# Kernel tuning notes

Hardware: AMD Instinct MI355X
Metric: run time of the kernel (lower is better)

The kernel has to match this reference:

```python
import jax, jax.numpy as jnp
import numpy as np

RATIO = 2          # BigVGAN Activation1d up/down ratio
K_FILT = 12        # int(6 * ratio // 2) * 2
DILATIONS = (1, 3, 5)


def _kaiser_sinc_filter1d(cutoff, half_width, kernel_size):
    # Faithful port of BigVGAN's kaiser_sinc_filter1d (even kernel path).
    half_size = kernel_size // 2
    delta_f = 4.0 * half_width
    A = 2.285 * (half_size - 1) * np.pi * delta_f + 7.95
    if A > 50.0:
        beta = 0.1102 * (A - 8.7)
    elif A >= 21.0:
        beta = 0.5842 * (A - 21.0) ** 0.4 + 0.07886 * (A - 21.0)
    else:
        beta = 0.0
    window = np.kaiser(kernel_size, beta)              # periodic=False
    time = np.arange(-half_size, half_size) + 0.5       # even kernel size
    filt = 2.0 * cutoff * window * np.sinc(2.0 * cutoff * time)
    filt = filt / filt.sum()
    return jnp.asarray(filt, dtype=jnp.float32)

FILT = _kaiser_sinc_filter1d(0.5 / RATIO, 0.6 / RATIO, K_FILT)


def _depthwise1d(x, filt, stride, lhs_dilation, padding):
    # x: (B, T, C), filt: (k,) shared across channels (depthwise)
    C = x.shape[-1]
    kern = jnp.tile(filt[:, None, None], (1, 1, C))  # (k, 1, C)
    return jax.lax.conv_general_dilated(
        x, kern, window_strides=(stride,), padding=padding,
        lhs_dilation=(lhs_dilation,), feature_group_count=C,
        dimension_numbers=('NLC', 'LIO', 'NLC'))


def upsample2(x):
    # BigVGAN UpSample1d(ratio=2): replicate pad -> conv_transpose -> crop
    pad = K_FILT // RATIO - 1                       # 5
    pad_left = pad * RATIO + (K_FILT - RATIO) // 2  # 15
    pad_right = pad * RATIO + (K_FILT - RATIO + 1) // 2  # 15
    x = jnp.pad(x, ((0, 0), (pad, pad), (0, 0)), mode='edge')
    # conv_transpose(stride=r) == lhs-dilated conv with full padding
    # (filter is symmetric, so no flip needed)
    y = RATIO * _depthwise1d(x, FILT, 1, RATIO, [(K_FILT - 1, K_FILT - 1)])
    return y[:, pad_left:-pad_right, :]  # (B, 2T, C)


def downsample2(x):
    # BigVGAN DownSample1d(ratio=2) == LowPassFilter1d(stride=2)
    pad_left = K_FILT // 2 - 1  # 5 (even kernel)
    pad_right = K_FILT // 2     # 6
    x = jnp.pad(x, ((0, 0), (pad_left, pad_right), (0, 0)), mode='edge')
    return _depthwise1d(x, FILT, RATIO, 1, 'VALID')  # (B, T, C)


def snake(x, log_alpha):
    # alpha_logscale=True: alpha = exp(param); x + (1/alpha) sin^2(alpha x)
    alpha = jnp.exp(log_alpha)  # (C,), broadcasts over (B, T, C)
    return x + (1.0 / (alpha + 1e-9)) * jnp.square(jnp.sin(alpha * x))


def act1d(x, log_alpha):
    return downsample2(snake(upsample2(x), log_alpha))


def wn_conv(x, v, g, b, dilation):
    # weight-norm: kernel = v / ||v||_(0,1) * g, then SAME dilated conv
    norm = jnp.linalg.norm(v, axis=(0, 1))[None, None, :]  # (1,1,Cout)
    kern = (v / norm) * g  # (k, Cin, Cout)
    y = jax.lax.conv_general_dilated(
        x, kern, window_strides=(1,), padding='SAME',
        rhs_dilation=(dilation,), dimension_numbers=('NLC', 'LIO', 'NLC'))
    return y + b


def setup_inputs() -> dict:
    key = jax.random.key(0)
    ks = jax.random.split(key, 7)
    B, T, C, K = 4, 8192, 512, 3
    n = len(DILATIONS)
    x = jax.random.normal(ks[0], (B, T, C), dtype=jnp.float32)
    v1 = jax.random.normal(ks[1], (n, K, C, C), dtype=jnp.float32)
    g1 = jax.random.uniform(ks[2], (n, 1, 1, C), dtype=jnp.float32)
    b1 = 0.01 * jax.random.normal(ks[3], (n, C), dtype=jnp.float32)
    v2 = jax.random.normal(ks[4], (n, K, C, C), dtype=jnp.float32)
    g2 = jax.random.uniform(ks[5], (n, 1, 1, C), dtype=jnp.float32)
    b2 = 0.01 * jax.random.normal(ks[6], (n, C), dtype=jnp.float32)
    alphas = jnp.zeros((2 * n, C), dtype=jnp.float32)  # log-alpha init 0
    return {'x': x, 'v1': v1, 'g1': g1, 'b1': b1,
            'v2': v2, 'g2': g2, 'b2': b2, 'alphas': alphas}


def reference(x, v1, g1, b1, v2, g2, b2, alphas):
    for i, d in enumerate(DILATIONS):
        xt = act1d(x, alphas[2 * i])
        xt = wn_conv(xt, v1[i], g1[i], b1[i], d)
        xt = act1d(xt, alphas[2 * i + 1])
        xt = wn_conv(xt, v2[i], g2[i], b2[i], 1)
        x = xt + x
    return x
```

## Files before the change

### kernel.cpp

```cpp
#include <hip/hip_runtime.h>
#include <math.h>

#define TLEN   8192
#define CCH    512
#define NBATCH 4
#define GUARD_B 8
#define GUARD_T 16
#define XROWS  (TLEN + GUARD_B + GUARD_T)

typedef __attribute__((ext_vector_type(8))) short short8;
typedef __attribute__((ext_vector_type(4))) float f32x4;

struct Filt { float f[12]; };

#define MFMA16(a, b, c) __builtin_amdgcn_mfma_f32_16x16x32_bf16(a, b, c, 0, 0, 0)
#define BARRIER() asm volatile("s_barrier" ::: "memory")
#define VMCNT(n)  asm volatile("s_waitcnt vmcnt(" #n ")" ::: "memory")

__device__ __forceinline__ unsigned short f2bf(float f) {
  unsigned u = __float_as_uint(f);
  unsigned r = (u + 0x7fffu + ((u >> 16) & 1u)) >> 16;
  return (unsigned short)r;
}

__device__ __forceinline__ float bf2f(unsigned short u) {
  return __uint_as_float((unsigned)u << 16);
}

__device__ __forceinline__ float fast_sin(float x) {
  float r = x * 0.15915494309189535f;
  r -= floorf(r);
  return __builtin_amdgcn_sinf(r);
}

__device__ __forceinline__ float snake1(float u, float a, float rcp) {
  float s = fast_sin(a * u);
  return fmaf(rcp * s, s, u);
}

__device__ __forceinline__ void gload16(const void* g, void* l) {
  __builtin_amdgcn_global_load_lds(
      (const __attribute__((address_space(1))) unsigned int*)g,
      (__attribute__((address_space(3))) unsigned int*)l, 16, 0, 0);
}

__global__ __launch_bounds__(256)
void normp_k(const float* __restrict__ v1, const float* __restrict__ v2,
             float* __restrict__ part) {
  __shared__ float red[256];
  const int c  = blockIdx.x;
  const int cc = blockIdx.y;
  const int jc = blockIdx.z;
  const int col = threadIdx.x & 63;
  const int js  = threadIdx.x >> 6;
  const int co = cc * 64 + col;
  const float* v = (c < 3) ? v1 + (size_t)c * 3 * CCH * CCH
                           : v2 + (size_t)(c - 3) * 3 * CCH * CCH;
  const int j0 = jc * 64 + js * 16;
  float s = 0.f;
  #pragma unroll
  for (int jj = 0; jj < 16; ++jj) {
    float w = v[(size_t)(j0 + jj) * CCH + co];
    s = fmaf(w, w, s);
  }
  red[threadIdx.x] = s;
  __syncthreads();
  if (threadIdx.x < 64) {
    float t = red[threadIdx.x] + red[threadIdx.x + 64] +
              red[threadIdx.x + 128] + red[threadIdx.x + 192];
    part[(size_t)(c * CCH + co) * 24 + jc] = t;
  }
}

__global__ __launch_bounds__(256)
void fin_k(const float* __restrict__ part, const float* __restrict__ g1,
           const float* __restrict__ g2, float* __restrict__ scl) {
  const int i = blockIdx.x * 256 + threadIdx.x;
  const int c = i >> 9, co = i & 511;
  float s = 0.f;
  #pragma unroll
  for (int jc = 0; jc < 24; ++jc) s += part[(size_t)i * 24 + jc];
  const float g = (c < 3) ? g1[c * CCH + co] : g2[(c - 3) * CCH + co];
  scl[i] = g / sqrtf(s);
}

__global__ __launch_bounds__(512)
void zguard_k(unsigned short* __restrict__ xb) {
  const int b = blockIdx.x / 24;
  const int g = blockIdx.x % 24;
  const int row = (g < 8) ? g : (TLEN + g);
  xb[((size_t)b * XROWS + row) * CCH + threadIdx.x] = 0;
}

__global__ __launch_bounds__(256)
void wprep_k(const float* __restrict__ v1, const float* __restrict__ v2,
             const float* __restrict__ scl, unsigned short* __restrict__ wp) {
  const int gtid = blockIdx.x * 256 + threadIdx.x;
  const int lane = gtid & 63;
  const int gw = gtid >> 6;
  const int c  = gw / 1536;
  const int r  = gw - c * 1536;
  const int s  = r >> 6;
  const int r2 = r & 63;
  const int coT = r2 >> 5;
  const int cb  = r2 & 31;
  const int tap = s % 3, cib = s / 3;
  const int nf = cb >> 1, kk = cb & 1;
  const int co  = coT * 256 + nf * 16 + (lane & 15);
  const int ci0 = cib * 64 + kk * 32 + (lane >> 4) * 8;
  const float* v = (c < 3) ? v1 + (size_t)c * 3 * CCH * CCH
                           : v2 + (size_t)(c - 3) * 3 * CCH * CCH;
  const float sc = scl[c * CCH + co];
  unsigned short o[8];
  #pragma unroll
  for (int j = 0; j < 8; ++j) {
    float w = v[((size_t)tap * CCH + ci0 + j) * CCH + co] * sc;
    o[j] = f2bf(w);
  }
  *reinterpret_cast<short8*>(wp + (size_t)gw * 512 + lane * 8) =
      *reinterpret_cast<const short8*>(o);
}

template<int INBF>
__global__ __launch_bounds__(256)
void act_k(const void* __restrict__ xin, unsigned short* __restrict__ y,
           const float* __restrict__ la, Filt F) {
  const int idx = blockIdx.x * 256 + threadIdx.x;
  const int c  = (idx & 127) << 2;
  const int ts = (idx >> 7) & 2047;
  const int b  = idx >> 18;
  const int t0 = ts * 4;

  auto ldrow = [&](int row) -> f32x4 {
    if constexpr (INBF) {
      const unsigned short* p =
          (const unsigned short*)xin + ((size_t)b * TLEN + row) * CCH + c;
      ushort4 u = *reinterpret_cast<const ushort4*>(p);
      f32x4 r;
      r[0] = bf2f(u.x); r[1] = bf2f(u.y); r[2] = bf2f(u.z); r[3] = bf2f(u.w);
      return r;
    } else {
      const float* p = (const float*)xin + ((size_t)b * TLEN + row) * CCH + c;
      return *reinterpret_cast<const f32x4*>(p);
    }
  };

  float av[4], rv[4];
  #pragma unroll
  for (int ch = 0; ch < 4; ++ch) {
    av[ch] = expf(la[c + ch]);
    rv[ch] = 1.f / (av[ch] + 1e-9f);
  }

  float acc[4][4];

  if (ts >= 2 && ts <= 2045) {
    f32x4 xw[14];
    #pragma unroll
    for (int j = 0; j < 14; ++j) xw[j] = ldrow(t0 - 5 + j);

    #pragma unroll
    for (int ch = 0; ch < 4; ++ch) {
      float s[18];
      #pragma unroll
      for (int mi = 0; mi < 18; ++mi) {
        float u = 0.f;
        if (mi & 1) {
          const int base = (mi - 5) / 2 + 2;
          #pragma unroll
          for (int r = 0; r < 6; ++r) u = fmaf(F.f[2*r], xw[base + r][ch], u);
        } else {
          const int base = (mi - 6) / 2 + 3;
          #pragma unroll
          for (int r = 0; r < 6; ++r) u = fmaf(F.f[2*r+1], xw[base + r][ch], u);
        }
        u *= 2.f;
        s[mi] = snake1(u, av[ch], rv[ch]);
      }
      #pragma unroll
      for (int tt = 0; tt < 4; ++tt) {
        float a = 0.f;
        #pragma unroll
        for (int k = 0; k < 12; ++k) a = fmaf(F.f[k], s[2*tt + k], a);
        acc[tt][ch] = a;
      }
    }
  } else {
    #pragma unroll
    for (int tt = 0; tt < 4; ++tt) {
      const int t = t0 + tt;
      float a0=0.f, a1=0.f, a2=0.f, a3=0.f;
      for (int k = 0; k < 12; ++k) {
        int m  = 2*t + k - 5;
        int mc = m < 0 ? 0 : (m > 2*TLEN - 1 ? 2*TLEN - 1 : m);
        int tp = mc >> 1;
        int odd = mc & 1;
        float u0=0.f,u1=0.f,u2=0.f,u3=0.f;
        #pragma unroll
        for (int r = 0; r < 6; ++r) {
          int i  = odd ? (tp + r - 2) : (tp + r - 3);
          int ic = i < 0 ? 0 : (i > TLEN - 1 ? TLEN - 1 : i);
          float tap = odd ? F.f[2*r+1] : F.f[2*r];
          f32x4 xv = ldrow(ic);
          u0 = fmaf(tap, xv[0], u0); u1 = fmaf(tap, xv[1], u1);
          u2 = fmaf(tap, xv[2], u2); u3 = fmaf(tap, xv[3], u3);
        }
        u0 *= 2.f; u1 *= 2.f; u2 *= 2.f; u3 *= 2.f;
        const float fk = F.f[k];
        a0 = fmaf(fk, snake1(u0,av[0],rv[0]), a0);
        a1 = fmaf(fk, snake1(u1,av[1],rv[1]), a1);
        a2 = fmaf(fk, snake1(u2,av[2],rv[2]), a2);
        a3 = fmaf(fk, snake1(u3,av[3],rv[3]), a3);
      }
      acc[tt][0]=a0; acc[tt][1]=a1; acc[tt][2]=a2; acc[tt][3]=a3;
    }
  }

  #pragma unroll
  for (int tt = 0; tt < 4; ++tt) {
    ushort4 o;
    o.x = f2bf(acc[tt][0]); o.y = f2bf(acc[tt][1]);
    o.z = f2bf(acc[tt][2]); o.w = f2bf(acc[tt][3]);
    *reinterpret_cast<ushort4*>(
        y + ((size_t)b * XROWS + GUARD_B + t0 + tt) * CCH + c) = o;
  }
}

template<int DIL, int MODE>
__global__ __launch_bounds__(512, 2)
void convm_k(const unsigned short* __restrict__ xb,
             const unsigned short* __restrict__ wp,
             const float* __restrict__ bia,
             const float* __restrict__ resf,
             const unsigned short* __restrict__ resb,
             float* __restrict__ outf,
             unsigned short* __restrict__ outb) {
  __shared__ unsigned short Abuf[2][2][128 * 64];
  __shared__ unsigned short Bbuf[2][2][16 * 512];

  const int tid  = threadIdx.x;
  const int lane = tid & 63;
  const int wid  = tid >> 6;
  const int wr   = wid >> 2;
  const int wcn  = wid & 3;

  const int l   = (blockIdx.x & 7) * 32 + (blockIdx.x >> 3);
  const int coT = l & 1;
  const int tb  = l >> 1;
  const int b   = tb >> 5;
  const int t0  = (tb & 31) * 256;
  const int co0 = coT * 256;

  const int qq = lane >> 4;
  const int r0 = lane & 15;
  const int xr = r0 & 7;

  const int a_r = lane >> 3;
  const int a_c = (lane & 7) ^ a_r;

  const unsigned short* xrow0 =
      xb + ((size_t)b * XROWS + GUARD_B + t0 - DIL) * CCH;
  const unsigned short* wpc = wp + (size_t)coT * 32 * 512 + lane * 8;

  f32x4 acc[8][4] = {};
  short8 bfr[4][2];

  auto stA = [&](int s, int h) {
    const int tap = s % 3, cib = s / 3;
    const unsigned short* base =
        xrow0 + (size_t)(tap * DIL + h * 128) * CCH + cib * 64;
    #pragma unroll
    for (int u = 0; u < 2; ++u) {
      const int i = wid * 2 + u;
      gload16(base + (size_t)(8 * i + a_r) * CCH + a_c * 8,
              &Abuf[s & 1][h][i * 512]);
    }
  };
  auto stB = [&](int s, int h) {
    #pragma unroll
    for (int u = 0; u < 2; ++u) {
      const int cbl = wid * 2 + u;
      gload16(wpc + ((size_t)s * 64 + h * 16 + cbl) * 512,
              &Bbuf[s & 1][h][cbl * 512]);
    }
  };
  auto ldB = [&](int slot) {
    const int hb = wcn >> 1;
    #pragma unroll
    for (int j = 0; j < 4; ++j)
      #pragma unroll
      for (int kk = 0; kk < 2; ++kk) {
        const int chunk = ((wcn & 1) * 4 + j) * 2 + kk;
        bfr[j][kk] = *reinterpret_cast<const short8*>(
            &Bbuf[slot][hb][chunk * 512 + lane * 8]);
      }
  };
  auto ldA = [&](int slot, int q, short8 (&af)[2][2]) {
    #pragma unroll
    for (int e = 0; e < 2; ++e) {
      const int row = q * 32 + e * 16 + r0;
      #pragma unroll
      for (int kk = 0; kk < 2; ++kk)
        af[e][kk] = *reinterpret_cast<const short8*>(
            &Abuf[slot][wr][row * 64 + ((kk * 4 + qq) ^ xr) * 8]);
    }
  };
  auto mma = [&](int q, short8 (&af)[2][2]) {
    __builtin_amdgcn_s_setprio(1);
    #pragma unroll
    for (int kk = 0; kk < 2; ++kk)
      #pragma unroll
      for (int e = 0; e < 2; ++e)
        #pragma unroll
        for (int j = 0; j < 4; ++j)
          acc[q * 2 + e][j] = MFMA16(af[e][kk], bfr[j][kk], acc[q * 2 + e][j]);
    __builtin_amdgcn_s_setprio(0);
  };

  stA(0, 0); stA(0, 1);
  stB(0, 0); stB(0, 1);
  stB(1, 0); stB(1, 1);
  VMCNT(4);
  BARRIER();

  for (int m = 0; m < 12; ++m) {
    const int s0 = 2 * m, s1 = 2 * m + 1;
    short8 af[2][2];
    ldB(0); ldA(0, 0, af); stA(s1, 0);
    BARRIER(); mma(0, af); BARRIER();
    ldA(0, 1, af); stA(s1, 1);
    BARRIER(); mma(1, af); BARRIER();
    ldA(0, 2, af); if (m < 11) stB(s0 + 2, 0);
    BARRIER(); mma(2, af); BARRIER();
    ldA(0, 3, af);
    if (m < 11) { stB(s0 + 2, 1); VMCNT(4); } else { VMCNT(0); }
    BARRIER(); mma(3, af); BARRIER();
    ldB(1); ldA(1, 0, af); if (m < 11) stA(s0 + 2, 0);
    BARRIER(); mma(0, af); BARRIER();
    ldA(1, 1, af); if (m < 11) stA(s0 + 2, 1);
    BARRIER(); mma(1, af); BARRIER();
    ldA(1, 2, af); if (m < 11) stB(s1 + 2, 0);
    BARRIER(); mma(2, af); BARRIER();
    ldA(1, 3, af);
    if (m < 11) { stB(s1 + 2, 1); VMCNT(4); }
    BARRIER(); mma(3, af); BARRIER();
  }

  #pragma unroll
  for (int j = 0; j < 4; ++j) {
    const int co = co0 + wcn * 64 + j * 16 + r0;
    const float bv = bia[co];
    #pragma unroll
    for (int i = 0; i < 8; ++i) {
      const int t = t0 + wr * 128 + i * 16 + qq * 4;
      #pragma unroll
      for (int e = 0; e < 4; ++e) {
        const size_t off = ((size_t)b * TLEN + t + e) * CCH + co;
        float o = acc[i][j][e] + bv;
        if constexpr (MODE == 1) o += resf[off];
        if constexpr (MODE == 2 || MODE == 3) o += bf2f(resb[off]);
        if constexpr (MODE == 3) outf[off] = o;
        else                     outb[off] = f2bf(o);
      }
    }
  }
}

static double bessel_i0(double x) {
  double t = 1.0, s = 1.0, q = x * x * 0.25;
  for (int k = 1; k < 64; ++k) {
    t *= q / ((double)k * (double)k);
    s += t;
    if (t < 1e-18 * s) break;
  }
  return s;
}

static void make_filter(Filt* F) {
  const double cutoff = 0.25, hw = 0.3;
  const int ks = 12, half = 6;
  const double A = 2.285 * (half - 1) * M_PI * (4.0 * hw) + 7.95;
  double beta;
  if (A > 50.0)       beta = 0.1102 * (A - 8.7);
  else if (A >= 21.0) beta = 0.5842 * pow(A - 21.0, 0.4) + 0.07886 * (A - 21.0);
  else                beta = 0.0;
  const double i0b = bessel_i0(beta);
  double f[12], sum = 0.0;
  for (int n = 0; n < 12; ++n) {
    double rr = 2.0 * n / (ks - 1) - 1.0;
    double w  = bessel_i0(beta * sqrt(fmax(0.0, 1.0 - rr * rr))) / i0b;
    double tm = (double)(n - half) + 0.5;
    double sx = 2.0 * cutoff * tm;
    double snc = (sx == 0.0) ? 1.0 : sin(M_PI * sx) / (M_PI * sx);
    f[n] = 2.0 * cutoff * w * snc;
    sum += f[n];
  }
  for (int n = 0; n < 12; ++n) F->f[n] = (float)(f[n] / sum);
}

extern "C" void kernel_launch(void* const* d_in, const int* in_sizes, int n_in,
                              void* d_out, int out_size, void* d_ws, size_t ws_size,
                              hipStream_t stream) {
  (void)in_sizes; (void)n_in; (void)out_size; (void)ws_size;
  const float* x  = (const float*)d_in[0];
  const float* v1 = (const float*)d_in[1];
  const float* g1 = (const float*)d_in[2];
  const float* b1 = (const float*)d_in[3];
  const float* v2 = (const float*)d_in[4];
  const float* g2 = (const float*)d_in[5];
  const float* b2 = (const float*)d_in[6];
  const float* al = (const float*)d_in[7];
  float* out = (float*)d_out;

  const size_t N = (size_t)NBATCH * TLEN * CCH;
  unsigned short* wb1  = (unsigned short*)d_ws;
  unsigned short* xbuf = wb1 + N;
  unsigned short* xres = xbuf + (size_t)NBATCH * XROWS * CCH;
  unsigned short* wp   = xres + N;
  float* part = (float*)(wp + (size_t)6 * 3 * CCH * CCH);
  float* scl  = part + (size_t)6 * CCH * 24;

  Filt F;
  make_filter(&F);

  zguard_k<<<96, 512, 0, stream>>>(xbuf);
  normp_k<<<dim3(6, 8, 24), 256, 0, stream>>>(v1, v2, part);
  fin_k<<<12, 256, 0, stream>>>(part, g1, g2, scl);
  wprep_k<<<2304, 256, 0, stream>>>(v1, v2, scl, wp);

  const int cgrid = NBATCH * (TLEN / 256) * 2;
  const int nblk_act = (NBATCH * 2048 * 128) / 256;
  const size_t wsz = (size_t)3 * CCH * CCH;

  act_k<0><<<nblk_act, 256, 0, stream>>>(x, xbuf, al + 0 * CCH, F);
  convm_k<1, 0><<<cgrid, 512, 0, stream>>>(xbuf, wp + 0 * wsz, b1 + 0 * CCH,
                                           nullptr, nullptr, nullptr, wb1);
  act_k<1><<<nblk_act, 256, 0, stream>>>(wb1, xbuf, al + 1 * CCH, F);
  convm_k<1, 1><<<cgrid, 512, 0, stream>>>(xbuf, wp + 3 * wsz, b2 + 0 * CCH,
                                           x, nullptr, nullptr, xres);

  act_k<1><<<nblk_act, 256, 0, stream>>>(xres, xbuf, al + 2 * CCH, F);
  convm_k<3, 0><<<cgrid, 512, 0, stream>>>(xbuf, wp + 1 * wsz, b1 + 1 * CCH,
                                           nullptr, nullptr, nullptr, wb1);
  act_k<1><<<nblk_act, 256, 0, stream>>>(wb1, xbuf, al + 3 * CCH, F);
  convm_k<1, 2><<<cgrid, 512, 0, stream>>>(xbuf, wp + 4 * wsz, b2 + 1 * CCH,
                                           nullptr, xres, nullptr, xres);

  act_k<1><<<nblk_act, 256, 0, stream>>>(xres, xbuf, al + 4 * CCH, F);
  convm_k<5, 0><<<cgrid, 512, 0, stream>>>(xbuf, wp + 2 * wsz, b1 + 2 * CCH,
                                           nullptr, nullptr, nullptr, wb1);
  act_k<1><<<nblk_act, 256, 0, stream>>>(wb1, xbuf, al + 5 * CCH, F);
  convm_k<1, 3><<<cgrid, 512, 0, stream>>>(xbuf, wp + 5 * wsz, b2 + 2 * CCH,
                                           nullptr, xres, out, nullptr);
}
```

Baseline: 673.2 us.

## Share one A halo tile across all three conv taps in convm kernel

The conv kernel used to reload a fresh 256-row A tile for every tap. It now loads one 272-row tile per input-channel block, including the dilation halo, and reads all three taps from it at shifted row offsets with an adjusted XOR swizzle. B weights move to a 5-slot ring buffer with a reordered packing layout, and the wait counts and stage order are rewritten to match. The aim is to cut A global loads roughly threefold, at the cost of more LDS use and a more fragile pipeline schedule.

```diff
diff --git a/kernel.cpp b/kernel.cpp
--- a/kernel.cpp
+++ b/kernel.cpp
@@ -102,11 +102,12 @@
   const int r  = gw - c * 1536;
   const int s  = r >> 6;
   const int r2 = r & 63;
-  const int coT = r2 >> 5;
-  const int cb  = r2 & 31;
+  const int coT  = r2 >> 5;
+  const int half = (r2 >> 4) & 1;
+  const int cb   = r2 & 15;
   const int tap = s % 3, cib = s / 3;
   const int nf = cb >> 1, kk = cb & 1;
-  const int co  = coT * 256 + nf * 16 + (lane & 15);
+  const int co  = coT * 256 + half * 128 + nf * 16 + (lane & 15);
   const int ci0 = cib * 64 + kk * 32 + (lane >> 4) * 8;
   const float* v = (c < 3) ? v1 + (size_t)c * 3 * CCH * CCH
                            : v2 + (size_t)(c - 3) * 3 * CCH * CCH;
@@ -235,14 +236,15 @@
              const unsigned short* __restrict__ resb,
              float* __restrict__ outf,
              unsigned short* __restrict__ outb) {
-  __shared__ unsigned short Abuf[2][2][128 * 64];
-  __shared__ unsigned short Bbuf[2][2][16 * 512];
+  __shared__ unsigned short Abuf[2][272 * 64];
+  __shared__ unsigned short Bbuf[5][16 * 512];
 
   const int tid  = threadIdx.x;
   const int lane = tid & 63;
   const int wid  = tid >> 6;
   const int wr   = wid >> 2;
   const int wcn  = wid & 3;
+  const int hb   = wcn >> 1;
 
   const int l   = (blockIdx.x & 7) * 32 + (blockIdx.x >> 3);
   const int coT = l & 1;
@@ -253,56 +255,53 @@
 
   const int qq = lane >> 4;
   const int r0 = lane & 15;
-  const int xr = r0 & 7;
 
   const int a_r = lane >> 3;
   const int a_c = (lane & 7) ^ a_r;
 
   const unsigned short* xrow0 =
-      xb + ((size_t)b * XROWS + GUARD_B + t0 - DIL) * CCH;
-  const unsigned short* wpc = wp + (size_t)coT * 32 * 512 + lane * 8;
+      xb + ((size_t)b * XROWS + GUARD_B + t0 - 8) * CCH;
+  const unsigned short* wpc = wp;
 
   f32x4 acc[8][4] = {};
   short8 bfr[4][2];
 
-  auto stA = [&](int s, int h) {
-    const int tap = s % 3, cib = s / 3;
-    const unsigned short* base =
-        xrow0 + (size_t)(tap * DIL + h * 128) * CCH + cib * 64;
-    #pragma unroll
-    for (int u = 0; u < 2; ++u) {
-      const int i = wid * 2 + u;
-      gload16(base + (size_t)(8 * i + a_r) * CCH + a_c * 8,
-              &Abuf[s & 1][h][i * 512]);
-    }
-  };
-  auto stB = [&](int s, int h) {
-    #pragma unroll
-    for (int u = 0; u < 2; ++u) {
-      const int cbl = wid * 2 + u;
-      gload16(wpc + ((size_t)s * 64 + h * 16 + cbl) * 512,
-              &Bbuf[s & 1][h][cbl * 512]);
-    }
-  };
-  auto ldB = [&](int slot) {
-    const int hb = wcn >> 1;
+  auto stA = [&](int cib, int i) {
+    int G;
+    if (i < 4) G = i * 8 + wid;
+    else       G = (wid >= 6) ? (26 + wid) : wid;
+    const unsigned short* g =
+        xrow0 + (size_t)(8 * G + a_r) * CCH + cib * 64 + a_c * 8;
+    gload16(g, &Abuf[cib & 1][G * 512]);
+  };
+  auto stB = [&](int s, int i) {
+    const int half = i >> 1, part = i & 1;
+    const int pos = (2 * s + half) % 5;
+    const unsigned short* g =
+        wpc + ((((size_t)s * 2 + coT) * 2 + half) * 16 + part * 8) * 512 + tid * 8;
+    gload16(g, &Bbuf[pos][part * 4096 + wid * 512]);
+  };
+  auto ldB = [&](int s) {
+    const int pos = (2 * s + hb) % 5;
     #pragma unroll
     for (int j = 0; j < 4; ++j)
       #pragma unroll
       for (int kk = 0; kk < 2; ++kk) {
         const int chunk = ((wcn & 1) * 4 + j) * 2 + kk;
         bfr[j][kk] = *reinterpret_cast<const short8*>(
-            &Bbuf[slot][hb][chunk * 512 + lane * 8]);
+            &Bbuf[pos][chunk * 512 + lane * 8]);
       }
   };
-  auto ldA = [&](int slot, int q, short8 (&af)[2][2]) {
+  auto ldA = [&](int pa, int tap, int q, short8 (&af)[2][2]) {
+    const int tapoff = 8 + (tap - 1) * DIL;
+    const int xr = (tapoff + r0) & 7;
     #pragma unroll
     for (int e = 0; e < 2; ++e) {
-      const int row = q * 32 + e * 16 + r0;
+      const int row = tapoff + wr * 128 + q * 32 + e * 16 + r0;
       #pragma unroll
       for (int kk = 0; kk < 2; ++kk)
         af[e][kk] = *reinterpret_cast<const short8*>(
-            &Abuf[slot][wr][row * 64 + ((kk * 4 + qq) ^ xr) * 8]);
+            &Abuf[pa][row * 64 + ((kk * 4 + qq) ^ xr) * 8]);
     }
   };
   auto mma = [&](int q, short8 (&af)[2][2]) {
@@ -317,32 +316,49 @@
     __builtin_amdgcn_s_setprio(0);
   };
 
-  stA(0, 0); stA(0, 1);
-  stB(0, 0); stB(0, 1);
-  stB(1, 0); stB(1, 1);
+  stA(0, 0); stB(0, 0); stA(0, 1); stB(0, 1);
+  stA(0, 2); stB(0, 2); stA(0, 3); stB(0, 3); stA(0, 4);
+  stB(1, 0); stB(1, 1); stB(1, 2); stB(1, 3);
   VMCNT(4);
   BARRIER();
 
-  for (int m = 0; m < 12; ++m) {
-    const int s0 = 2 * m, s1 = 2 * m + 1;
+  for (int c = 0; c < 8; ++c) {
+    const int T = 3 * c;
+    const int pa = c & 1;
     short8 af[2][2];
-    ldB(0); ldA(0, 0, af); stA(s1, 0);
+    const bool more = (c < 7);
+
+    ldB(T);
+    ldA(pa, 0, 0, af); stB(T + 2, 0);
     BARRIER(); mma(0, af); BARRIER();
-    ldA(0, 1, af); stA(s1, 1);
+    ldA(pa, 0, 1, af); stB(T + 2, 1);
     BARRIER(); mma(1, af); BARRIER();
-    ldA(0, 2, af); if (m < 11) stB(s0 + 2, 0);
+    ldA(pa, 0, 2, af); stB(T + 2, 2);
     BARRIER(); mma(2, af); BARRIER();
-    ldA(0, 3, af);
-    if (m < 11) { stB(s0 + 2, 1); VMCNT(4); } else { VMCNT(0); }
+    ldA(pa, 0, 3, af); stB(T + 2, 3);
+    VMCNT(4);
     BARRIER(); mma(3, af); BARRIER();
-    ldB(1); ldA(1, 0, af); if (m < 11) stA(s0 + 2, 0);
+
+    ldB(T + 1);
+    ldA(pa, 1, 0, af); if (more) { stB(T + 3, 0); stA(c + 1, 0); }
     BARRIER(); mma(0, af); BARRIER();
-    ldA(1, 1, af); if (m < 11) stA(s0 + 2, 1);
+    ldA(pa, 1, 1, af); if (more) { stB(T + 3, 1); stA(c + 1, 1); }
     BARRIER(); mma(1, af); BARRIER();
-    ldA(1, 2, af); if (m < 11) stB(s1 + 2, 0);
+    ldA(pa, 1, 2, af); if (more) { stB(T + 3, 2); stA(c + 1, 2); }
     BARRIER(); mma(2, af); BARRIER();
-    ldA(1, 3, af);
-    if (m < 11) { stB(s1 + 2, 1); VMCNT(4); }
+    ldA(pa, 1, 3, af); if (more) { stB(T + 3, 3); stA(c + 1, 3); }
+    if (more) { VMCNT(8); } else { VMCNT(0); }
+    BARRIER(); mma(3, af); BARRIER();
+
+    ldB(T + 2);
+    ldA(pa, 2, 0, af); if (more) { stA(c + 1, 4); stB(T + 4, 0); }
+    BARRIER(); mma(0, af); BARRIER();
+    ldA(pa, 2, 1, af); if (more) stB(T + 4, 1);
+    BARRIER(); mma(1, af); BARRIER();
+    ldA(pa, 2, 2, af); if (more) stB(T + 4, 2);
+    BARRIER(); mma(2, af); BARRIER();
+    ldA(pa, 2, 3, af);
+    if (more) { stB(T + 4, 3); VMCNT(4); }
     BARRIER(); mma(3, af); BARRIER();
   }
 
```

Result: faster. 648.0 us (median of 2 runs) (-3.8%).

## Restructure conv GEMM into barrier-free per-wave tiles with halo A reuse across taps

Applied to the files above, without the earlier changes.

The conv kernel moves from 512-thread blocks with shared, barrier-synchronised A and B tiles to 256-thread blocks where each wave owns a private double-buffered A halo tile (140 rows x 32 channels). All three taps are computed from that one halo tile, and weights are read straight from global into registers. The weight prepack layout changes to match the new 64-column per-wave grouping. This drops block barriers and the redundant per-tap A loads, but B is now fetched uncached from global by every wave, and the global loads are no longer shared across the block.

```diff
diff --git a/kernel.cpp b/kernel.cpp
--- a/kernel.cpp
+++ b/kernel.cpp
@@ -14,7 +14,6 @@
 struct Filt { float f[12]; };
 
 #define MFMA16(a, b, c) __builtin_amdgcn_mfma_f32_16x16x32_bf16(a, b, c, 0, 0, 0)
-#define BARRIER() asm volatile("s_barrier" ::: "memory")
 #define VMCNT(n)  asm volatile("s_waitcnt vmcnt(" #n ")" ::: "memory")
 
 __device__ __forceinline__ unsigned short f2bf(float f) {
@@ -100,22 +99,21 @@
   const int gw = gtid >> 6;
   const int c  = gw / 1536;
   const int r  = gw - c * 1536;
-  const int s  = r >> 6;
-  const int r2 = r & 63;
-  const int coT = r2 >> 5;
-  const int cb  = r2 & 31;
-  const int tap = s % 3, cib = s / 3;
-  const int nf = cb >> 1, kk = cb & 1;
-  const int co  = coT * 256 + nf * 16 + (lane & 15);
-  const int ci0 = cib * 64 + kk * 32 + (lane >> 4) * 8;
+  const int s  = r >> 5;
+  const int r2 = r & 31;
+  const int g8 = r2 >> 2;
+  const int j  = r2 & 3;
+  const int tap = s % 3, c16 = s / 3;
+  const int co  = g8 * 64 + j * 16 + (lane & 15);
+  const int ci0 = c16 * 32 + (lane >> 4) * 8;
   const float* v = (c < 3) ? v1 + (size_t)c * 3 * CCH * CCH
                            : v2 + (size_t)(c - 3) * 3 * CCH * CCH;
   const float sc = scl[c * CCH + co];
   unsigned short o[8];
   #pragma unroll
-  for (int j = 0; j < 8; ++j) {
-    float w = v[((size_t)tap * CCH + ci0 + j) * CCH + co] * sc;
-    o[j] = f2bf(w);
+  for (int jj = 0; jj < 8; ++jj) {
+    float w = v[((size_t)tap * CCH + ci0 + jj) * CCH + co] * sc;
+    o[jj] = f2bf(w);
   }
   *reinterpret_cast<short8*>(wp + (size_t)gw * 512 + lane * 8) =
       *reinterpret_cast<const short8*>(o);
@@ -227,7 +225,7 @@
 }
 
 template<int DIL, int MODE>
-__global__ __launch_bounds__(512, 2)
+__global__ __launch_bounds__(256, 2)
 void convm_k(const unsigned short* __restrict__ xb,
              const unsigned short* __restrict__ wp,
              const float* __restrict__ bia,
@@ -235,124 +233,86 @@
              const unsigned short* __restrict__ resb,
              float* __restrict__ outf,
              unsigned short* __restrict__ outb) {
-  __shared__ unsigned short Abuf[2][2][128 * 64];
-  __shared__ unsigned short Bbuf[2][2][16 * 512];
+  __shared__ unsigned short Abuf[4][2][140 * 32];
 
   const int tid  = threadIdx.x;
   const int lane = tid & 63;
-  const int wid  = tid >> 6;
-  const int wr   = wid >> 2;
-  const int wcn  = wid & 3;
-
-  const int l   = (blockIdx.x & 7) * 32 + (blockIdx.x >> 3);
-  const int coT = l & 1;
-  const int tb  = l >> 1;
+  const int w    = tid >> 6;
+  const int wr   = w >> 1;
+  const int wc   = w & 1;
+
+  const int l   = (blockIdx.x & 7) * 64 + (blockIdx.x >> 3);
+  const int coB = l & 3;
+  const int tb  = l >> 2;
   const int b   = tb >> 5;
-  const int t0  = (tb & 31) * 256;
-  const int co0 = coT * 256;
+  const int t0w = (tb & 31) * 256 + wr * 128;
+  const int co0 = coB * 128 + wc * 64;
+  const int g8  = coB * 2 + wc;
 
   const int qq = lane >> 4;
   const int r0 = lane & 15;
-  const int xr = r0 & 7;
-
-  const int a_r = lane >> 3;
-  const int a_c = (lane & 7) ^ a_r;
-
-  const unsigned short* xrow0 =
-      xb + ((size_t)b * XROWS + GUARD_B + t0 - DIL) * CCH;
-  const unsigned short* wpc = wp + (size_t)coT * 32 * 512 + lane * 8;
+  const int a_r = lane >> 2;
+  const int a_c = lane & 3;
+
+  const unsigned short* xw0 =
+      xb + ((size_t)b * XROWS + GUARD_B + t0w - 6) * CCH;
+  unsigned short* const As0 = &Abuf[w][0][0];
+  unsigned short* const As1 = &Abuf[w][1][0];
 
   f32x4 acc[8][4] = {};
-  short8 bfr[4][2];
-
-  auto stA = [&](int s, int h) {
-    const int tap = s % 3, cib = s / 3;
-    const unsigned short* base =
-        xrow0 + (size_t)(tap * DIL + h * 128) * CCH + cib * 64;
-    #pragma unroll
-    for (int u = 0; u < 2; ++u) {
-      const int i = wid * 2 + u;
-      gload16(base + (size_t)(8 * i + a_r) * CCH + a_c * 8,
-              &Abuf[s & 1][h][i * 512]);
+
+  auto stA = [&](int c16, unsigned short* dst) {
+    #pragma unroll
+    for (int i = 0; i < 9; ++i) {
+      const int rb = (i < 8) ? 16 * i : 124;
+      const int R  = rb + a_r;
+      const int sc = a_c ^ ((R >> 1) & 3);
+      gload16(xw0 + (size_t)R * CCH + c16 * 32 + sc * 8, dst + rb * 32);
     }
   };
-  auto stB = [&](int s, int h) {
-    #pragma unroll
-    for (int u = 0; u < 2; ++u) {
-      const int cbl = wid * 2 + u;
-      gload16(wpc + ((size_t)s * 64 + h * 16 + cbl) * 512,
-              &Bbuf[s & 1][h][cbl * 512]);
-    }
-  };
-  auto ldB = [&](int slot) {
-    const int hb = wcn >> 1;
-    #pragma unroll
-    for (int j = 0; j < 4; ++j)
-      #pragma unroll
-      for (int kk = 0; kk < 2; ++kk) {
-        const int chunk = ((wcn & 1) * 4 + j) * 2 + kk;
-        bfr[j][kk] = *reinterpret_cast<const short8*>(
-            &Bbuf[slot][hb][chunk * 512 + lane * 8]);
+
+  stA(0, As0);
+
+  for (int c16 = 0; c16 < 16; ++c16) {
+    VMCNT(0);
+    const unsigned short* Ab = (c16 & 1) ? As1 : As0;
+    if (c16 < 15) stA(c16 + 1, (c16 & 1) ? As0 : As1);
+
+    #pragma unroll
+    for (int tap = 0; tap < 3; ++tap) {
+      const int s = c16 * 3 + tap;
+      const unsigned short* wb =
+          wp + (((size_t)s * 8 + g8) * 4) * 512 + lane * 8;
+      short8 bf[4];
+      #pragma unroll
+      for (int j = 0; j < 4; ++j)
+        bf[j] = *reinterpret_cast<const short8*>(wb + (size_t)j * 512);
+
+      const int rbase = 6 + (tap - 1) * DIL;
+      short8 af[8];
+      #pragma unroll
+      for (int i = 0; i < 8; ++i) {
+        const int row = rbase + i * 16 + r0;
+        af[i] = *reinterpret_cast<const short8*>(
+            Ab + row * 32 + (qq ^ ((row >> 1) & 3)) * 8);
       }
-  };
-  auto ldA = [&](int slot, int q, short8 (&af)[2][2]) {
-    #pragma unroll
-    for (int e = 0; e < 2; ++e) {
-      const int row = q * 32 + e * 16 + r0;
-      #pragma unroll
-      for (int kk = 0; kk < 2; ++kk)
-        af[e][kk] = *reinterpret_cast<const short8*>(
-            &Abuf[slot][wr][row * 64 + ((kk * 4 + qq) ^ xr) * 8]);
-    }
-  };
-  auto mma = [&](int q, short8 (&af)[2][2]) {
-    __builtin_amdgcn_s_setprio(1);
-    #pragma unroll
-    for (int kk = 0; kk < 2; ++kk)
-      #pragma unroll
-      for (int e = 0; e < 2; ++e)
+      __builtin_amdgcn_s_setprio(1);
+      #pragma unroll
+      for (int i = 0; i < 8; ++i)
         #pragma unroll
         for (int j = 0; j < 4; ++j)
-          acc[q * 2 + e][j] = MFMA16(af[e][kk], bfr[j][kk], acc[q * 2 + e][j]);
-    __builtin_amdgcn_s_setprio(0);
-  };
-
-  stA(0, 0); stA(0, 1);
-  stB(0, 0); stB(0, 1);
-  stB(1, 0); stB(1, 1);
-  VMCNT(4);
-  BARRIER();
-
-  for (int m = 0; m < 12; ++m) {
-    const int s0 = 2 * m, s1 = 2 * m + 1;
-    short8 af[2][2];
-    ldB(0); ldA(0, 0, af); stA(s1, 0);
-    BARRIER(); mma(0, af); BARRIER();
-    ldA(0, 1, af); stA(s1, 1);
-    BARRIER(); mma(1, af); BARRIER();
-    ldA(0, 2, af); if (m < 11) stB(s0 + 2, 0);
-    BARRIER(); mma(2, af); BARRIER();
-    ldA(0, 3, af);
-    if (m < 11) { stB(s0 + 2, 1); VMCNT(4); } else { VMCNT(0); }
-    BARRIER(); mma(3, af); BARRIER();
-    ldB(1); ldA(1, 0, af); if (m < 11) stA(s0 + 2, 0);
-    BARRIER(); mma(0, af); BARRIER();
-    ldA(1, 1, af); if (m < 11) stA(s0 + 2, 1);
-    BARRIER(); mma(1, af); BARRIER();
-    ldA(1, 2, af); if (m < 11) stB(s1 + 2, 0);
-    BARRIER(); mma(2, af); BARRIER();
-    ldA(1, 3, af);
-    if (m < 11) { stB(s1 + 2, 1); VMCNT(4); }
-    BARRIER(); mma(3, af); BARRIER();
+          acc[i][j] = MFMA16(af[i], bf[j], acc[i][j]);
+      __builtin_amdgcn_s_setprio(0);
+    }
   }
 
   #pragma unroll
   for (int j = 0; j < 4; ++j) {
-    const int co = co0 + wcn * 64 + j * 16 + r0;
+    const int co = co0 + j * 16 + r0;
     const float bv = bia[co];
     #pragma unroll
     for (int i = 0; i < 8; ++i) {
-      const int t = t0 + wr * 128 + i * 16 + qq * 4;
+      const int t = t0w + i * 16 + qq * 4;
       #pragma unroll
       for (int e = 0; e < 4; ++e) {
         const size_t off = ((size_t)b * TLEN + t + e) * CCH + co;
@@ -428,28 +388,28 @@
   fin_k<<<12, 256, 0, stream>>>(part, g1, g2, scl);
   wprep_k<<<2304, 256, 0, stream>>>(v1, v2, scl, wp);
 
-  const int cgrid = NBATCH * (TLEN / 256) * 2;
+  const int cgrid = NBATCH * (TLEN / 256) * 4;
   const int nblk_act = (NBATCH * 2048 * 128) / 256;
   const size_t wsz = (size_t)3 * CCH * CCH;
 
   act_k<0><<<nblk_act, 256, 0, stream>>>(x, xbuf, al + 0 * CCH, F);
-  convm_k<1, 0><<<cgrid, 512, 0, stream>>>(xbuf, wp + 0 * wsz, b1 + 0 * CCH,
+  convm_k<1, 0><<<cgrid, 256, 0, stream>>>(xbuf, wp + 0 * wsz, b1 + 0 * CCH,
                                            nullptr, nullptr, nullptr, wb1);
   act_k<1><<<nblk_act, 256, 0, stream>>>(wb1, xbuf, al + 1 * CCH, F);
-  convm_k<1, 1><<<cgrid, 512, 0, stream>>>(xbuf, wp + 3 * wsz, b2 + 0 * CCH,
+  convm_k<1, 1><<<cgrid, 256, 0, stream>>>(xbuf, wp + 3 * wsz, b2 + 0 * CCH,
                                            x, nullptr, nullptr, xres);
 
   act_k<1><<<nblk_act, 256, 0, stream>>>(xres, xbuf, al + 2 * CCH, F);
-  convm_k<3, 0><<<cgrid, 512, 0, stream>>>(xbuf, wp + 1 * wsz, b1 + 1 * CCH,
+  convm_k<3, 0><<<cgrid, 256, 0, stream>>>(xbuf, wp + 1 * wsz, b1 + 1 * CCH,
                                            nullptr, nullptr, nullptr, wb1);
   act_k<1><<<nblk_act, 256, 0, stream>>>(wb1, xbuf, al + 3 * CCH, F);
-  convm_k<1, 2><<<cgrid, 512, 0, stream>>>(xbuf, wp + 4 * wsz, b2 + 1 * CCH,
+  convm_k<1, 2><<<cgrid, 256, 0, stream>>>(xbuf, wp + 4 * wsz, b2 + 1 * CCH,
                                            nullptr, xres, nullptr, xres);
 
   act_k<1><<<nblk_act, 256, 0, stream>>>(xres, xbuf, al + 4 * CCH, F);
-  convm_k<5, 0><<<cgrid, 512, 0, stream>>>(xbuf, wp + 2 * wsz, b1 + 2 * CCH,
+  convm_k<5, 0><<<cgrid, 256, 0, stream>>>(xbuf, wp + 2 * wsz, b1 + 2 * CCH,
                                            nullptr, nullptr, nullptr, wb1);
   act_k<1><<<nblk_act, 256, 0, stream>>>(wb1, xbuf, al + 5 * CCH, F);
-  convm_k<1, 3><<<cgrid, 512, 0, stream>>>(xbuf, wp + 5 * wsz, b2 + 2 * CCH,
+  convm_k<1, 3><<<cgrid, 256, 0, stream>>>(xbuf, wp + 5 * wsz, b2 + 2 * CCH,
                                            nullptr, xres, out, nullptr);
 }
```

Measured after the change: 651.6 us. 1.03x faster.
